# Performance work log

Hardware: AMD Instinct MI355X
Metric: run time of the kernel (lower is better)

## Reference

```python
import jax, jax.numpy as jnp
import numpy as np

B, D, C = 32, 30, 4        # batch, input spatial, in-channels
KS = 3                     # kernel size per dim
OD = D - KS + 1            # 28 (valid padding, stride 1)
P = OD ** 3                # 21952 output positions
K = (KS ** 3) * C          # 108 taps per output position
F = 4                      # output filters


def _patches(x):
    # x: [B, D, D, D, C] -> [B, P, K]
    xt = jnp.transpose(x, (0, 4, 1, 2, 3))  # NCDHW
    p = jax.lax.conv_general_dilated_patches(
        xt, filter_shape=(KS, KS, KS), window_strides=(1, 1, 1), padding='VALID')
    # p: [B, C*KS^3, OD, OD, OD]
    p = jnp.transpose(p, (0, 2, 3, 4, 1))
    return p.reshape(p.shape[0], P, K)


def _local_conv(x, W):
    # Locally-connected 3D conv (unshared weights) == structured sparse matmul.
    # W: [P, K, F] one weight per (output position, tap, filter).
    return jnp.einsum('bpk,pkf->bpf', _patches(x), W)


def setup_inputs() -> dict:
    key = jax.random.key(0)
    ks = jax.random.split(key, 7)
    x = jax.random.normal(ks[0], (B, D, D, D, C), jnp.float32)
    kernel_loc = jax.random.normal(ks[1], (P, K, F), jnp.float32) * 0.05
    kernel_rho = jax.random.normal(ks[2], (P, K, F), jnp.float32) * 0.1 - 5.0  # softplus -> small scale
    bias = jax.random.normal(ks[3], (F,), jnp.float32) * 0.05
    eps = jax.random.normal(ks[4], (P, K, F), jnp.float32)
    sign_in = jax.random.rademacher(ks[5], (B, D, D, D, C), jnp.float32)
    sign_out = jax.random.rademacher(ks[6], (B, P, F), jnp.float32)
    return dict(x=x, kernel_loc=kernel_loc, kernel_rho=kernel_rho, bias=bias,
                eps=eps, sign_in=sign_in, sign_out=sign_out)


def reference(x, kernel_loc, kernel_rho, bias, eps, sign_in, sign_out):
    # Flipout estimator: deterministic mean path + sign-perturbed noise path.
    scale = jax.nn.softplus(kernel_rho)
    out = _local_conv(x, kernel_loc)                                  # [B, P, F]
    out = out + sign_out * _local_conv(x * sign_in, scale * eps)      # flipout perturbation
    out = out + bias                                                  # per-filter bias (channels_last)
    return out.reshape(x.shape[0], OD, OD, OD, F)
```

## Files before the change

kernel.cpp:

```cpp
#include <hip/hip_runtime.h>


constexpr int Bn   = 32;
constexpr int Dn   = 30;
constexpr int Cn   = 4;
constexpr int ODn  = 28;
constexpr int Pn   = ODn * ODn * ODn;
constexpr int Tt   = 27;
constexpr int Kn   = Tt * Cn;
constexpr int Fn   = 4;
constexpr int PPB  = 8;
constexpr int THREADS = 256;

__global__ __launch_bounds__(THREADS) void lc3d_flipout_kernel(
    const float* __restrict__ x,
    const float* __restrict__ loc,
    const float* __restrict__ rho,
    const float* __restrict__ bias,
    const float* __restrict__ eps,
    const float* __restrict__ sgn_in,
    const float* __restrict__ sgn_out,
    float* __restrict__ out)
{
    __shared__ float4 wm[PPB * Tt * Cn];
    __shared__ float4 wn[PPB * Tt * Cn];

    const int tid    = threadIdx.x;
    const int p_base = blockIdx.x * PPB;

    const float4* loc4 = (const float4*)loc + (size_t)p_base * Kn;
    const float4* rho4 = (const float4*)rho + (size_t)p_base * Kn;
    const float4* eps4 = (const float4*)eps + (size_t)p_base * Kn;

    for (int g = tid; g < PPB * Kn; g += THREADS) {
        const int p_loc = g / Kn;
        const int rem   = g - p_loc * Kn;
        const int c     = rem / Tt;
        const int t     = rem - c * Tt;
        const float4 L = loc4[g];
        const float4 R = rho4[g];
        const float4 E = eps4[g];
        float4 W;
        W.x = (R.x > 15.f ? R.x : __logf(1.f + __expf(R.x))) * E.x;
        W.y = (R.y > 15.f ? R.y : __logf(1.f + __expf(R.y))) * E.y;
        W.z = (R.z > 15.f ? R.z : __logf(1.f + __expf(R.z))) * E.z;
        W.w = (R.w > 15.f ? R.w : __logf(1.f + __expf(R.w))) * E.w;
        const int l = p_loc * Kn + t * Cn + c;
        wm[l] = L;
        wn[l] = W;
    }
    __syncthreads();

    const int b     = tid & 31;
    const int p_loc = tid >> 5;
    const int p     = p_base + p_loc;
    const int od    = p / (ODn * ODn);
    const int prem  = p - od * (ODn * ODn);
    const int oh    = prem / ODn;
    const int ow    = prem - oh * ODn;

    const size_t vox = (((size_t)b * Dn + od) * Dn + oh) * Dn + ow;
    const float4* xb = (const float4*)x      + vox;
    const float4* sb = (const float4*)sgn_in + vox;
    const float4* wmp = wm + p_loc * Kn;
    const float4* wnp = wn + p_loc * Kn;

    float am0 = 0.f, am1 = 0.f, am2 = 0.f, am3 = 0.f;
    float an0 = 0.f, an1 = 0.f, an2 = 0.f, an3 = 0.f;

    #pragma unroll
    for (int kd = 0; kd < 3; ++kd) {
        #pragma unroll
        for (int kh = 0; kh < 3; ++kh) {
            const float4* xr = xb + (kd * Dn + kh) * Dn;
            const float4* sr = sb + (kd * Dn + kh) * Dn;
            #pragma unroll
            for (int kw = 0; kw < 3; ++kw) {
                const int t = (kd * 3 + kh) * 3 + kw;
                const float4 xv = xr[kw];
                const float4 sv = sr[kw];
                const float4 m0 = wmp[t * Cn + 0];
                const float4 m1 = wmp[t * Cn + 1];
                const float4 m2 = wmp[t * Cn + 2];
                const float4 m3 = wmp[t * Cn + 3];
                const float4 n0 = wnp[t * Cn + 0];
                const float4 n1 = wnp[t * Cn + 1];
                const float4 n2 = wnp[t * Cn + 2];
                const float4 n3 = wnp[t * Cn + 3];

                am0 = fmaf(xv.x, m0.x, am0); am0 = fmaf(xv.y, m1.x, am0);
                am0 = fmaf(xv.z, m2.x, am0); am0 = fmaf(xv.w, m3.x, am0);
                am1 = fmaf(xv.x, m0.y, am1); am1 = fmaf(xv.y, m1.y, am1);
                am1 = fmaf(xv.z, m2.y, am1); am1 = fmaf(xv.w, m3.y, am1);
                am2 = fmaf(xv.x, m0.z, am2); am2 = fmaf(xv.y, m1.z, am2);
                am2 = fmaf(xv.z, m2.z, am2); am2 = fmaf(xv.w, m3.z, am2);
                am3 = fmaf(xv.x, m0.w, am3); am3 = fmaf(xv.y, m1.w, am3);
                am3 = fmaf(xv.z, m2.w, am3); am3 = fmaf(xv.w, m3.w, am3);

                const float xs0 = xv.x * sv.x;
                const float xs1 = xv.y * sv.y;
                const float xs2 = xv.z * sv.z;
                const float xs3 = xv.w * sv.w;

                an0 = fmaf(xs0, n0.x, an0); an0 = fmaf(xs1, n1.x, an0);
                an0 = fmaf(xs2, n2.x, an0); an0 = fmaf(xs3, n3.x, an0);
                an1 = fmaf(xs0, n0.y, an1); an1 = fmaf(xs1, n1.y, an1);
                an1 = fmaf(xs2, n2.y, an1); an1 = fmaf(xs3, n3.y, an1);
                an2 = fmaf(xs0, n0.z, an2); an2 = fmaf(xs1, n1.z, an2);
                an2 = fmaf(xs2, n2.z, an2); an2 = fmaf(xs3, n3.z, an2);
                an3 = fmaf(xs0, n0.w, an3); an3 = fmaf(xs1, n1.w, an3);
                an3 = fmaf(xs2, n2.w, an3); an3 = fmaf(xs3, n3.w, an3);
            }
        }
    }

    const size_t ob = (size_t)b * Pn + p;
    const float4 so = ((const float4*)sgn_out)[ob];
    const float4 bi = *(const float4*)bias;
    float4 o;
    o.x = fmaf(so.x, an0, am0) + bi.x;
    o.y = fmaf(so.y, an1, am1) + bi.y;
    o.z = fmaf(so.z, an2, am2) + bi.z;
    o.w = fmaf(so.w, an3, am3) + bi.w;
    ((float4*)out)[ob] = o;
}

extern "C" void kernel_launch(void* const* d_in, const int* in_sizes, int n_in,
                              void* d_out, int out_size, void* d_ws, size_t ws_size,
                              hipStream_t stream) {
    const float* x    = (const float*)d_in[0];
    const float* loc  = (const float*)d_in[1];
    const float* rho  = (const float*)d_in[2];
    const float* bias = (const float*)d_in[3];
    const float* eps  = (const float*)d_in[4];
    const float* si   = (const float*)d_in[5];
    const float* so   = (const float*)d_in[6];
    float* out = (float*)d_out;

    lc3d_flipout_kernel<<<dim3(Pn / PPB), dim3(THREADS), 0, stream>>>(
        x, loc, rho, bias, eps, si, so, out);
}
```

Measured before the change: 237.4 us.

## Pack weights as bf16 in shared memory and compute two batches per thread

Mean and noise weights are stored in LDS as packed bf16 pairs, one uint4 per tap-channel with a padded stride. This halves LDS footprint and read traffic and lets each block hold 16 positions. Each thread now handles two batch elements per position, so every weight read from LDS is reused across two inputs. Rounding weights to bf16 lowers accuracy and may exceed tolerance, and the new thread mapping changes global access coalescing (16 consecutive positions per batch row).

```diff
diff --git a/kernel.cpp b/kernel.cpp
--- a/kernel.cpp
+++ b/kernel.cpp
@@ -8,11 +8,18 @@
 constexpr int Pn   = ODn * ODn * ODn;
 constexpr int Tt   = 27;
 constexpr int Kn   = Tt * Cn;
-constexpr int Fn   = 4;
-constexpr int PPB  = 8;
+constexpr int PPB  = 16;
 constexpr int THREADS = 256;
+constexpr int WSTRIDE = Kn + 1;
 
-__global__ __launch_bounds__(THREADS) void lc3d_flipout_kernel(
+__device__ __forceinline__ unsigned bf16rne(float f) {
+    unsigned u = __float_as_uint(f);
+    return (u + 0x7fffu + ((u >> 16) & 1u)) >> 16;
+}
+__device__ __forceinline__ float bflo(unsigned u) { return __uint_as_float(u << 16); }
+__device__ __forceinline__ float bfhi(unsigned u) { return __uint_as_float(u & 0xffff0000u); }
+
+__global__ __launch_bounds__(THREADS, 5) void lc3d_flipout_kernel(
     const float* __restrict__ x,
     const float* __restrict__ loc,
     const float* __restrict__ rho,
@@ -22,8 +29,7 @@
     const float* __restrict__ sgn_out,
     float* __restrict__ out)
 {
-    __shared__ float4 wm[PPB * Tt * Cn];
-    __shared__ float4 wn[PPB * Tt * Cn];
+    __shared__ uint4 w[PPB * WSTRIDE];
 
     const int tid    = threadIdx.x;
     const int p_base = blockIdx.x * PPB;
@@ -33,96 +39,104 @@
     const float4* eps4 = (const float4*)eps + (size_t)p_base * Kn;
 
     for (int g = tid; g < PPB * Kn; g += THREADS) {
-        const int p_loc = g / Kn;
-        const int rem   = g - p_loc * Kn;
-        const int c     = rem / Tt;
-        const int t     = rem - c * Tt;
+        const int pl = g / Kn;
+        const int k  = g - pl * Kn;
         const float4 L = loc4[g];
         const float4 R = rho4[g];
         const float4 E = eps4[g];
-        float4 W;
-        W.x = (R.x > 15.f ? R.x : __logf(1.f + __expf(R.x))) * E.x;
-        W.y = (R.y > 15.f ? R.y : __logf(1.f + __expf(R.y))) * E.y;
-        W.z = (R.z > 15.f ? R.z : __logf(1.f + __expf(R.z))) * E.z;
-        W.w = (R.w > 15.f ? R.w : __logf(1.f + __expf(R.w))) * E.w;
-        const int l = p_loc * Kn + t * Cn + c;
-        wm[l] = L;
-        wn[l] = W;
+        float nx = (R.x > 15.f ? R.x : __logf(1.f + __expf(R.x))) * E.x;
+        float ny = (R.y > 15.f ? R.y : __logf(1.f + __expf(R.y))) * E.y;
+        float nz = (R.z > 15.f ? R.z : __logf(1.f + __expf(R.z))) * E.z;
+        float nw = (R.w > 15.f ? R.w : __logf(1.f + __expf(R.w))) * E.w;
+        uint4 pk;
+        pk.x = bf16rne(L.x) | (bf16rne(L.y) << 16);
+        pk.y = bf16rne(L.z) | (bf16rne(L.w) << 16);
+        pk.z = bf16rne(nx)  | (bf16rne(ny) << 16);
+        pk.w = bf16rne(nz)  | (bf16rne(nw) << 16);
+        w[pl * WSTRIDE + k] = pk;
     }
     __syncthreads();
 
-    const int b     = tid & 31;
-    const int p_loc = tid >> 5;
-    const int p     = p_base + p_loc;
-    const int od    = p / (ODn * ODn);
-    const int prem  = p - od * (ODn * ODn);
-    const int oh    = prem / ODn;
-    const int ow    = prem - oh * ODn;
+    const int pl = tid & 15;
+    const int bh = tid >> 4;
+    const int b0 = bh, b1 = bh + 16;
+    const int p  = p_base + pl;
+    const int od   = p / (ODn * ODn);
+    const int prem = p - od * (ODn * ODn);
+    const int oh   = prem / ODn;
+    const int ow   = prem - oh * ODn;
 
-    const size_t vox = (((size_t)b * Dn + od) * Dn + oh) * Dn + ow;
-    const float4* xb = (const float4*)x      + vox;
-    const float4* sb = (const float4*)sgn_in + vox;
-    const float4* wmp = wm + p_loc * Kn;
-    const float4* wnp = wn + p_loc * Kn;
+    const float4* x4 = (const float4*)x;
+    const float4* s4 = (const float4*)sgn_in;
+    const size_t v0 = (((size_t)b0 * Dn + od) * Dn + oh) * Dn + ow;
+    const size_t v1 = (((size_t)b1 * Dn + od) * Dn + oh) * Dn + ow;
+    const uint4* wp = w + pl * WSTRIDE;
 
-    float am0 = 0.f, am1 = 0.f, am2 = 0.f, am3 = 0.f;
-    float an0 = 0.f, an1 = 0.f, an2 = 0.f, an3 = 0.f;
+    float a00=0.f,a01=0.f,a02=0.f,a03=0.f;
+    float a10=0.f,a11=0.f,a12=0.f,a13=0.f;
+    float n00=0.f,n01=0.f,n02=0.f,n03=0.f;
+    float n10=0.f,n11=0.f,n12=0.f,n13=0.f;
+
+#define CHAN(c, xa_c, sa_c, xb_c, sb_c)                                      \
+    {                                                                        \
+        const uint4 wv = wp[(c) * Tt + t];                                   \
+        const float m0 = bflo(wv.x), m1 = bfhi(wv.x);                        \
+        const float m2 = bflo(wv.y), m3 = bfhi(wv.y);                        \
+        const float q0 = bflo(wv.z), q1 = bfhi(wv.z);                        \
+        const float q2 = bflo(wv.w), q3 = bfhi(wv.w);                        \
+        a00 = fmaf(xa_c, m0, a00); a01 = fmaf(xa_c, m1, a01);                \
+        a02 = fmaf(xa_c, m2, a02); a03 = fmaf(xa_c, m3, a03);                \
+        a10 = fmaf(xb_c, m0, a10); a11 = fmaf(xb_c, m1, a11);                \
+        a12 = fmaf(xb_c, m2, a12); a13 = fmaf(xb_c, m3, a13);                \
+        const float ya = (xa_c) * (sa_c);                                    \
+        const float yb = (xb_c) * (sb_c);                                    \
+        n00 = fmaf(ya, q0, n00); n01 = fmaf(ya, q1, n01);                    \
+        n02 = fmaf(ya, q2, n02); n03 = fmaf(ya, q3, n03);                    \
+        n10 = fmaf(yb, q0, n10); n11 = fmaf(yb, q1, n11);                    \
+        n12 = fmaf(yb, q2, n12); n13 = fmaf(yb, q3, n13);                    \
+    }
 
     #pragma unroll
     for (int kd = 0; kd < 3; ++kd) {
         #pragma unroll
         for (int kh = 0; kh < 3; ++kh) {
-            const float4* xr = xb + (kd * Dn + kh) * Dn;
-            const float4* sr = sb + (kd * Dn + kh) * Dn;
+            const int roff = (kd * Dn + kh) * Dn;
+            const float4* xr0 = x4 + v0 + roff;
+            const float4* sr0 = s4 + v0 + roff;
+            const float4* xr1 = x4 + v1 + roff;
+            const float4* sr1 = s4 + v1 + roff;
             #pragma unroll
             for (int kw = 0; kw < 3; ++kw) {
                 const int t = (kd * 3 + kh) * 3 + kw;
-                const float4 xv = xr[kw];
-                const float4 sv = sr[kw];
-                const float4 m0 = wmp[t * Cn + 0];
-                const float4 m1 = wmp[t * Cn + 1];
-                const float4 m2 = wmp[t * Cn + 2];
-                const float4 m3 = wmp[t * Cn + 3];
-                const float4 n0 = wnp[t * Cn + 0];
-                const float4 n1 = wnp[t * Cn + 1];
-                const float4 n2 = wnp[t * Cn + 2];
-                const float4 n3 = wnp[t * Cn + 3];
-
-                am0 = fmaf(xv.x, m0.x, am0); am0 = fmaf(xv.y, m1.x, am0);
-                am0 = fmaf(xv.z, m2.x, am0); am0 = fmaf(xv.w, m3.x, am0);
-                am1 = fmaf(xv.x, m0.y, am1); am1 = fmaf(xv.y, m1.y, am1);
-                am1 = fmaf(xv.z, m2.y, am1); am1 = fmaf(xv.w, m3.y, am1);
-                am2 = fmaf(xv.x, m0.z, am2); am2 = fmaf(xv.y, m1.z, am2);
-                am2 = fmaf(xv.z, m2.z, am2); am2 = fmaf(xv.w, m3.z, am2);
-                am3 = fmaf(xv.x, m0.w, am3); am3 = fmaf(xv.y, m1.w, am3);
-                am3 = fmaf(xv.z, m2.w, am3); am3 = fmaf(xv.w, m3.w, am3);
-
-                const float xs0 = xv.x * sv.x;
-                const float xs1 = xv.y * sv.y;
-                const float xs2 = xv.z * sv.z;
-                const float xs3 = xv.w * sv.w;
-
-                an0 = fmaf(xs0, n0.x, an0); an0 = fmaf(xs1, n1.x, an0);
-                an0 = fmaf(xs2, n2.x, an0); an0 = fmaf(xs3, n3.x, an0);
-                an1 = fmaf(xs0, n0.y, an1); an1 = fmaf(xs1, n1.y, an1);
-                an1 = fmaf(xs2, n2.y, an1); an1 = fmaf(xs3, n3.y, an1);
-                an2 = fmaf(xs0, n0.z, an2); an2 = fmaf(xs1, n1.z, an2);
-                an2 = fmaf(xs2, n2.z, an2); an2 = fmaf(xs3, n3.z, an2);
-                an3 = fmaf(xs0, n0.w, an3); an3 = fmaf(xs1, n1.w, an3);
-                an3 = fmaf(xs2, n2.w, an3); an3 = fmaf(xs3, n3.w, an3);
+                const float4 xa = xr0[kw];
+                const float4 sa = sr0[kw];
+                const float4 xb = xr1[kw];
+                const float4 sb = sr1[kw];
+                CHAN(0, xa.x, sa.x, xb.x, sb.x);
+                CHAN(1, xa.y, sa.y, xb.y, sb.y);
+                CHAN(2, xa.z, sa.z, xb.z, sb.z);
+                CHAN(3, xa.w, sa.w, xb.w, sb.w);
             }
         }
     }
+#undef CHAN
 
-    const size_t ob = (size_t)b * Pn + p;
-    const float4 so = ((const float4*)sgn_out)[ob];
     const float4 bi = *(const float4*)bias;
-    float4 o;
-    o.x = fmaf(so.x, an0, am0) + bi.x;
-    o.y = fmaf(so.y, an1, am1) + bi.y;
-    o.z = fmaf(so.z, an2, am2) + bi.z;
-    o.w = fmaf(so.w, an3, am3) + bi.w;
-    ((float4*)out)[ob] = o;
+    const size_t ob0 = (size_t)b0 * Pn + p;
+    const size_t ob1 = (size_t)b1 * Pn + p;
+    const float4 so0 = ((const float4*)sgn_out)[ob0];
+    const float4 so1 = ((const float4*)sgn_out)[ob1];
+    float4 o0, o1;
+    o0.x = fmaf(so0.x, n00, a00) + bi.x;
+    o0.y = fmaf(so0.y, n01, a01) + bi.y;
+    o0.z = fmaf(so0.z, n02, a02) + bi.z;
+    o0.w = fmaf(so0.w, n03, a03) + bi.w;
+    o1.x = fmaf(so1.x, n10, a10) + bi.x;
+    o1.y = fmaf(so1.y, n11, a11) + bi.y;
+    o1.z = fmaf(so1.z, n12, a12) + bi.z;
+    o1.w = fmaf(so1.w, n13, a13) + bi.w;
+    ((float4*)out)[ob0] = o0;
+    ((float4*)out)[ob1] = o1;
 }
 
 extern "C" void kernel_launch(void* const* d_in, const int* in_sizes, int n_in,
```

After: 721.8 us. +204.0%, slower.
